# Kernel tuning notes

Measured on AMD Instinct MI355X. Metric: run time of the kernel, lower is better.

The kernel has to match this reference:

```python
import jax, jax.numpy as jnp
import numpy as np

BETA = 0.25


def setup_inputs() -> dict:
    key = jax.random.key(0)
    k1, k2, k3, k4 = jax.random.split(key, 4)
    B, D, T, H, W = 2, 256, 8, 32, 32
    K = 8192
    z = jax.random.normal(k1, (B, D, T, H, W), dtype=jnp.float32)
    # nn.init.normal_(embedding.weight, mean=0, std=emb_dim ** -0.5)
    emb_w = jax.random.normal(k2, (K, D), dtype=jnp.float32) * (D ** -0.5)
    # torch Linear default init ~ U(-1/sqrt(in), 1/sqrt(in)); scaled normal is fine for a reference
    w1 = jax.random.normal(k3, (D, D), dtype=jnp.float32) * (D ** -0.5)
    w2 = jax.random.normal(k4, (D, D), dtype=jnp.float32) * (D ** -0.5)
    return {"z": z, "emb_w": emb_w, "w1": w1, "w2": w2}


def reference(z, emb_w, w1, w2):
    B, D, T, H, W = z.shape
    K = emb_w.shape[0]
    # permute to channels-last and flatten: [B,T,H,W,D] -> [N,D]
    z_cl = jnp.transpose(z, (0, 2, 3, 4, 1))
    z_flat = z_cl.reshape(-1, D)
    N = z_flat.shape[0]
    # simvq: Linear -> GELU (exact) -> Linear, both bias-free
    quant_codebook = jax.nn.gelu(emb_w @ w1.T, approximate=False) @ w2.T  # [K, D]
    # pairwise squared L2 distances [N, K]
    d = (
        jnp.sum(z_flat ** 2, axis=1, keepdims=True)
        + jnp.sum(quant_codebook ** 2, axis=1)
        - 2.0 * (z_flat @ quant_codebook.T)
    )
    mean_distance = jnp.mean(d)
    idx = jnp.argmin(d, axis=1)  # [N]
    # gather == one-hot @ codebook
    z_q_flat = quant_codebook[idx]  # [N, D]
    z_q = z_q_flat.reshape(z_cl.shape)
    # VQ loss with stop-gradients
    loss = jnp.mean((jax.lax.stop_gradient(z_q) - z_cl) ** 2) + BETA * jnp.mean(
        (z_q - jax.lax.stop_gradient(z_cl)) ** 2
    )
    # straight-through estimator
    z_q = z_cl + jax.lax.stop_gradient(z_q - z_cl)
    # perplexity from code usage histogram (== mean of one-hot encodings)
    counts = jnp.zeros((K,), dtype=jnp.float32).at[idx].add(1.0)
    e_mean = counts / N
    perplexity = jnp.exp(-jnp.sum(e_mean * jnp.log(e_mean + 1e-10)))
    # back to channels-first [B, D, T, H, W]
    z_q = jnp.transpose(z_q, (0, 4, 1, 2, 3))
    return z_q, loss, perplexity, mean_distance
```

## Files before the change

kernel.cpp:

```cpp
#include <hip/hip_runtime.h>
#include <math.h>

#define BATCH 2
#define DIM   256
#define THW   8192
#define NTOK  16384
#define KCB   8192
#define OUTQ  4194304
#define CAP   2000000
#define SCAP  5600

typedef short short8 __attribute__((ext_vector_type(8)));
typedef float f32x4 __attribute__((ext_vector_type(4)));

__device__ __forceinline__ unsigned short f2bf_rn(float v) {
    unsigned u = __float_as_uint(v);
    unsigned r = u + 0x7FFFu + ((u >> 16) & 1u);
    return (unsigned short)(r >> 16);
}
__device__ __forceinline__ float bf2f(unsigned short b) {
    return __uint_as_float((unsigned)b << 16);
}
__device__ __forceinline__ void gl2lds16(const unsigned short* g, unsigned short* l) {
    __builtin_amdgcn_global_load_lds(
        (const __attribute__((address_space(1))) void*)g,
        (__attribute__((address_space(3))) void*)l, 16, 0, 0);
}

__global__ void k_buildA(const float* __restrict__ z,
                         unsigned short* __restrict__ Ahi,
                         unsigned short* __restrict__ Alo,
                         float* __restrict__ zsq,
                         float* __restrict__ sA, float* __restrict__ sB,
                         float* __restrict__ partialZ) {
    __shared__ ushort2 tile[64][65];
    __shared__ float zacc[64];
    __shared__ float lacc[64];
    __shared__ float pz[256];
    int t = threadIdx.x;
    int n0 = blockIdx.x * 64;
    int b = n0 >> 13;
    int thw0 = n0 & 8191;
    if (t < 64) { zacc[t] = 0.f; lacc[t] = 0.f; }
    pz[t] = 0.f;
    __syncthreads();
    int nn_r = t & 63, dg = t >> 6;
    float a1 = 0.f, a2 = 0.f;
    for (int dc = 0; dc < 256; dc += 64) {
        for (int r = 0; r < 16; ++r) {
            int dd = r * 4 + dg;
            float v = z[((size_t)(b * 256 + dc + dd)) * 8192 + thw0 + nn_r];
            unsigned short hb = f2bf_rn(v);
            float hf = bf2f(hb);
            unsigned short lb = f2bf_rn(v - hf);
            float lf = bf2f(lb);
            tile[dd][nn_r] = make_ushort2(hb, lb);
            a1 += v * v;
            a2 += lf * lf;
        }
        __syncthreads();
        int kk = t & 63, ng = t >> 6;
        float dimsum = 0.f;
        for (int i2 = 0; i2 < 16; ++i2) {
            int nn = ng + i2 * 4;
            ushort2 hl = tile[kk][nn];
            size_t base = (size_t)(n0 + nn) * 256;
            Ahi[base + dc + kk] = hl.x;
            Alo[base + dc + kk] = hl.y;
            dimsum += bf2f(hl.x) + bf2f(hl.y);
        }
        atomicAdd(&pz[dc + kk], dimsum);
        __syncthreads();
    }
    atomicAdd(&zacc[nn_r], a1);
    atomicAdd(&lacc[nn_r], a2);
    __syncthreads();
    if (t < 64) {
        zsq[n0 + t] = zacc[t];
        sA[n0 + t] = 2.1f * sqrtf(lacc[t]);
        sB[n0 + t] = 2.1f * sqrtf(zacc[t]);
    }
    partialZ[blockIdx.x * 256 + t] = pz[t];
}

__global__ void k_splitW(const float* __restrict__ w1, const float* __restrict__ w2,
                         unsigned short* __restrict__ W1s, unsigned short* __restrict__ W2s) {
    int bid = blockIdx.x;
    int row = bid & 255;
    const float* src = (bid >> 8) ? w2 : w1;
    unsigned short* dst = ((bid >> 8) ? W2s : W1s) + (size_t)row * 768;
    int t = threadIdx.x;
    float v = src[row * 256 + t];
    unsigned short hb = f2bf_rn(v);
    unsigned short lb = f2bf_rn(v - bf2f(hb));
    dst[t] = hb;
    dst[256 + t] = hb;
    dst[512 + t] = lb;
}

__global__ void k_buildE(const float* __restrict__ emb, unsigned short* __restrict__ E) {
    int t = threadIdx.x;
    int row = blockIdx.x * 4 + (t >> 6);
    int e4 = (t & 63) * 4;
    float4 v = *(const float4*)&emb[(size_t)row * 256 + e4];
    ushort4 hi, lo;
    hi.x = f2bf_rn(v.x); lo.x = f2bf_rn(v.x - bf2f(hi.x));
    hi.y = f2bf_rn(v.y); lo.y = f2bf_rn(v.y - bf2f(hi.y));
    hi.z = f2bf_rn(v.z); lo.z = f2bf_rn(v.z - bf2f(hi.z));
    hi.w = f2bf_rn(v.w); lo.w = f2bf_rn(v.w - bf2f(hi.w));
    size_t base = (size_t)row * 768;
    *(ushort4*)&E[base + e4] = hi;
    *(ushort4*)&E[base + 256 + e4] = lo;
    *(ushort4*)&E[base + 512 + e4] = hi;
}

template <int GELU>
__global__ __launch_bounds__(256) void k_mlp(const unsigned short* __restrict__ A,
                                             const unsigned short* __restrict__ B,
                                             unsigned short* __restrict__ Hs,
                                             float* __restrict__ C_t) {
    __shared__ __align__(16) char smem[32768];
    unsigned short* Asm = (unsigned short*)smem;
    unsigned short* Bsm = (unsigned short*)(smem + 16384);

    int t = threadIdx.x;
    int lane = t & 63;
    int w = t >> 6;
    int wm = w >> 1, wn = w & 1;
    int m0 = blockIdx.y * 128;
    int n0 = blockIdx.x * 128;

    int rA = w * 8 + (lane >> 3);
    int ch_l = lane & 7;
    int ch_g = ch_l ^ (lane >> 3);
    const unsigned short* gA = A + (size_t)(m0 + rA) * 768 + ch_g * 8;
    const unsigned short* gB = B + (size_t)(n0 + rA) * 768 + ch_g * 8;
    unsigned short* lA = &Asm[rA * 64 + ch_l * 8];
    unsigned short* lB = &Bsm[rA * 64 + ch_l * 8];

    f32x4 acc[4][4];
#pragma unroll
    for (int i = 0; i < 4; ++i)
#pragma unroll
        for (int j = 0; j < 4; ++j)
            acc[i][j] = f32x4{0.f, 0.f, 0.f, 0.f};

#pragma unroll
    for (int i = 0; i < 4; ++i) {
        gl2lds16(gA + (size_t)(32 * i) * 768, lA + 32 * i * 64);
        gl2lds16(gB + (size_t)(32 * i) * 768, lB + 32 * i * 64);
    }
    __syncthreads();

    int l15 = lane & 15;
    int quad = lane >> 4;
    int sw = l15 & 7;
    for (int kc = 0; kc < 12; ++kc) {
#pragma unroll
        for (int kk = 0; kk < 2; ++kk) {
            short8 a[4], b[4];
#pragma unroll
            for (int i = 0; i < 4; ++i)
                a[i] = *(const short8*)&Asm[(wm * 64 + i * 16 + l15) * 64 +
                                            (((kk * 4 + quad) ^ sw) * 8)];
#pragma unroll
            for (int j = 0; j < 4; ++j)
                b[j] = *(const short8*)&Bsm[(wn * 64 + j * 16 + l15) * 64 +
                                            (((kk * 4 + quad) ^ sw) * 8)];
#pragma unroll
            for (int i = 0; i < 4; ++i)
#pragma unroll
                for (int j = 0; j < 4; ++j)
                    acc[i][j] = __builtin_amdgcn_mfma_f32_16x16x32_bf16(a[i], b[j], acc[i][j], 0, 0, 0);
        }
        __syncthreads();
        if (kc < 11) {
            int ko = (kc + 1) * 64;
#pragma unroll
            for (int i = 0; i < 4; ++i) {
                gl2lds16(gA + (size_t)(32 * i) * 768 + ko, lA + 32 * i * 64);
                gl2lds16(gB + (size_t)(32 * i) * 768 + ko, lB + 32 * i * 64);
            }
            __syncthreads();
        }
    }

#pragma unroll
    for (int i = 0; i < 4; ++i) {
#pragma unroll
        for (int reg = 0; reg < 4; ++reg) {
            int mrow = m0 + wm * 64 + i * 16 + quad * 4 + reg;
#pragma unroll
            for (int j = 0; j < 4; ++j) {
                int ncol = n0 + wn * 64 + j * 16 + l15;
                float h = acc[i][j][reg];
                if (GELU) {
                    float g = 0.5f * h * (1.f + erff(h * 0.70710678118654752f));
                    unsigned short hb = f2bf_rn(g);
                    unsigned short lb = f2bf_rn(g - bf2f(hb));
                    size_t base = (size_t)mrow * 768;
                    Hs[base + ncol] = hb;
                    Hs[base + 256 + ncol] = lb;
                    Hs[base + 512 + ncol] = hb;
                } else {
                    C_t[(size_t)mrow * 8192 + ncol] = h;
                }
            }
        }
    }
}

__global__ void k_buildB(const float* __restrict__ C_t,
                         unsigned short* __restrict__ Bhi,
                         unsigned short* __restrict__ Blo,
                         float* __restrict__ csq,
                         float* __restrict__ sC, float* __restrict__ sCl,
                         unsigned* __restrict__ tileMaxC, unsigned* __restrict__ tileMaxCl,
                         float* __restrict__ accums, float* __restrict__ partialC) {
    __shared__ ushort2 tile[64][65];
    __shared__ float kacc[64];
    __shared__ float lacc[64];
    __shared__ float pc[256];
    int t = threadIdx.x;
    int k0 = blockIdx.x * 64;
    if (t < 64) { kacc[t] = 0.f; lacc[t] = 0.f; }
    pc[t] = 0.f;
    __syncthreads();
    int nn_r = t & 63, dg = t >> 6;
    float a1 = 0.f, a2 = 0.f;
    for (int dc = 0; dc < 256; dc += 64) {
        for (int r = 0; r < 16; ++r) {
            int dd = r * 4 + dg;
            float v = C_t[(size_t)(dc + dd) * KCB + k0 + nn_r];
            unsigned short hb = f2bf_rn(v);
            float hf = bf2f(hb);
            unsigned short lb = f2bf_rn(v - hf);
            float lf = bf2f(lb);
            tile[dd][nn_r] = make_ushort2(hb, lb);
            a1 += v * v;
            a2 += lf * lf;
        }
        __syncthreads();
        int kk = t & 63, ng = t >> 6;
        float dimsum = 0.f;
        for (int i2 = 0; i2 < 16; ++i2) {
            int nn = ng + i2 * 4;
            ushort2 hl = tile[kk][nn];
            size_t base = (size_t)(k0 + nn) * 256;
            Bhi[base + dc + kk] = hl.x;
            Blo[base + dc + kk] = hl.y;
            dimsum += bf2f(hl.x) + bf2f(hl.y);
        }
        atomicAdd(&pc[dc + kk], dimsum);
        __syncthreads();
    }
    atomicAdd(&kacc[nn_r], a1);
    atomicAdd(&lacc[nn_r], a2);
    __syncthreads();
    if (t < 64) {
        float c2 = kacc[t], l2 = lacc[t];
        float sc = sqrtf(c2), sl = sqrtf(l2);
        csq[k0 + t] = c2;
        sC[k0 + t] = sc;
        sCl[k0 + t] = sl;
        int tl = blockIdx.x >> 1;
        atomicMax(&tileMaxC[tl], __float_as_uint(sc));
        atomicMax(&tileMaxCl[tl], __float_as_uint(sl));
        atomicMax((unsigned*)&accums[3], __float_as_uint(c2));
        atomicMax((unsigned*)&accums[4], __float_as_uint(l2));
    }
    partialC[blockIdx.x * 256 + t] = pc[t];
}

__global__ __launch_bounds__(512, 2) void k_dist_hi(const unsigned short* __restrict__ A,
                                                    const unsigned short* __restrict__ B,
                                                    const float* __restrict__ zsq,
                                                    const float* __restrict__ csq,
                                                    const float* __restrict__ sA,
                                                    const float* __restrict__ sB,
                                                    const unsigned* __restrict__ tileMaxC,
                                                    const unsigned* __restrict__ tileMaxCl,
                                                    unsigned long long* __restrict__ packed,
                                                    float* __restrict__ accums,
                                                    unsigned long long* __restrict__ cand) {
    __shared__ __align__(16) char smem[131072];
    float* sbd     = (float*)smem;
    float* gprev_s = (float*)(smem + 2048);
    float* thr     = (float*)(smem + 3072);
    unsigned* scnt  = (unsigned*)(smem + 4096);
    unsigned* sbase = (unsigned*)(smem + 4100);
    unsigned long long* scand = (unsigned long long*)(smem + 4112);

    int t = threadIdx.x;
    int lane = t & 63;
    int w = t >> 6;
    int wm = w >> 1, wn = w & 1;
    int m0 = blockIdx.x * 256;
    int n0 = blockIdx.y * 256;

    int rA0 = w * 8 + (lane >> 3);
    int ch_l = lane & 7;
    int ch_g = ch_l ^ (lane >> 3);
    const unsigned short* gA = A + (size_t)(m0 + rA0) * 256 + ch_g * 8;
    const unsigned short* gB = B + (size_t)(n0 + rA0) * 256 + ch_g * 8;
    unsigned short* smemU = (unsigned short*)smem;
    unsigned short* lA = smemU + rA0 * 64 + ch_l * 8;
    unsigned short* lB = smemU + 16384 + rA0 * 64 + ch_l * 8;

    int l15 = lane & 15;
    int quad = lane >> 4;
    int sw = l15 & 7;

    float M1 = sqrtf(accums[3]);
    float M2 = sqrtf(accums[4]);
    float msC  = fmaxf(__uint_as_float(tileMaxC[2 * blockIdx.y]),
                       __uint_as_float(tileMaxC[2 * blockIdx.y + 1]));
    float msCl = fmaxf(__uint_as_float(tileMaxCl[2 * blockIdx.y]),
                       __uint_as_float(tileMaxCl[2 * blockIdx.y + 1]));
    float cv[8];
    int cols[8];
#pragma unroll
    for (int j = 0; j < 8; ++j) {
        int cloc = wn * 128 + j * 16 + l15;
        cols[j] = n0 + cloc;
        cv[j] = csq[cols[j]];
    }

    f32x4 acc[4][8];
#pragma unroll
    for (int i = 0; i < 4; ++i)
#pragma unroll
        for (int j = 0; j < 8; ++j)
            acc[i][j] = f32x4{0.f, 0.f, 0.f, 0.f};

#pragma unroll
    for (int i = 0; i < 4; ++i)
        gl2lds16(gA + (size_t)(64 * i) * 256, lA + 64 * i * 64);
#pragma unroll
    for (int i = 0; i < 4; ++i)
        gl2lds16(gB + (size_t)(64 * i) * 256, lB + 64 * i * 64);
    __syncthreads();

    int cur = 0;
    for (int kc = 0; kc < 4; ++kc) {
        if (kc < 3) {
            int ko = (kc + 1) * 64;
            int nb = (cur ^ 1) * 32768;
#pragma unroll
            for (int i = 0; i < 4; ++i)
                gl2lds16(gA + (size_t)(64 * i) * 256 + ko, lA + nb + 64 * i * 64);
#pragma unroll
            for (int i = 0; i < 4; ++i)
                gl2lds16(gB + (size_t)(64 * i) * 256 + ko, lB + nb + 64 * i * 64);
        }
        const unsigned short* Ar = smemU + cur * 32768;
        const unsigned short* Br = smemU + cur * 32768 + 16384;
#pragma unroll
        for (int kk = 0; kk < 2; ++kk) {
            short8 a[4], b[8];
#pragma unroll
            for (int i = 0; i < 4; ++i)
                a[i] = *(const short8*)&Ar[(wm * 64 + i * 16 + l15) * 64 +
                                            (((kk * 4 + quad) ^ sw) * 8)];
#pragma unroll
            for (int j = 0; j < 8; ++j)
                b[j] = *(const short8*)&Br[(wn * 128 + j * 16 + l15) * 64 +
                                            (((kk * 4 + quad) ^ sw) * 8)];
#pragma unroll
            for (int i = 0; i < 4; ++i)
#pragma unroll
                for (int j = 0; j < 8; ++j)
                    acc[i][j] = __builtin_amdgcn_mfma_f32_16x16x32_bf16(a[i], b[j], acc[i][j], 0, 0, 0);
        }
        __syncthreads();
        cur ^= 1;
    }

    if (t == 0) *scnt = 0;
    if (t < 256) {
        const unsigned* hp = (const unsigned*)&packed[m0 + t];
        gprev_s[t] = __uint_as_float(__atomic_load_n(hp + 1, __ATOMIC_RELAXED));
    }
#pragma unroll
    for (int i = 0; i < 4; ++i) {
#pragma unroll
        for (int reg = 0; reg < 4; ++reg) {
            int rloc = wm * 64 + i * 16 + quad * 4 + reg;
            float zs = zsq[m0 + rloc];
            float bd = 3.4e38f;
#pragma unroll
            for (int j = 0; j < 8; ++j) {
                float d = (zs + cv[j]) - 2.0f * acc[i][j][reg];
                acc[i][j][reg] = d;
                bd = fminf(bd, d);
            }
#pragma unroll
            for (int off = 1; off < 16; off <<= 1)
                bd = fminf(bd, __shfl_xor(bd, off, 64));
            if (l15 == 0) sbd[wn * 256 + rloc] = bd;
        }
    }
    __syncthreads();
    if (t < 256) {
        float bd = fminf(sbd[t], sbd[256 + t]);
        atomicMin(&packed[m0 + t], (unsigned long long)__float_as_uint(bd) << 32);
        float g = fminf(bd, gprev_s[t]);
        thr[t] = g + 1e-3f + sA[m0 + t] * (M1 + msC) + sB[m0 + t] * (M2 + msCl);
    }
    __syncthreads();
    unsigned* cnt = (unsigned*)&accums[2];
#pragma unroll
    for (int i = 0; i < 4; ++i) {
#pragma unroll
        for (int reg = 0; reg < 4; ++reg) {
            int rloc = wm * 64 + i * 16 + quad * 4 + reg;
            float tr = thr[rloc];
            bool p[8];
            bool any = false;
#pragma unroll
            for (int j = 0; j < 8; ++j) {
                p[j] = acc[i][j][reg] <= tr;
                any |= p[j];
            }
            if (__ballot(any)) {
                unsigned rbits = (unsigned)((m0 + rloc) << 13);
#pragma unroll
                for (int j = 0; j < 8; ++j) {
                    if (p[j]) {
                        unsigned long long entry =
                            ((unsigned long long)__float_as_uint(acc[i][j][reg]) << 32) |
                            (rbits | (unsigned)cols[j]);
                        unsigned pos = atomicAdd(scnt, 1u);
                        if (pos < SCAP) scand[pos] = entry;
                        else {
                            unsigned gp2 = atomicAdd(cnt, 1u);
                            if (gp2 < CAP) cand[gp2] = entry;
                        }
                    }
                }
            }
        }
    }
    __syncthreads();
    if (t == 0) {
        unsigned m = *scnt;
        if (m > SCAP) m = SCAP;
        *scnt = m;
        *sbase = atomicAdd(cnt, m);
    }
    __syncthreads();
    {
        unsigned m = *scnt, b0 = *sbase;
        for (unsigned u = t; u < m; u += 512)
            if (b0 + u < CAP) cand[b0 + u] = scand[u];
    }
}

__global__ __launch_bounds__(256) void k_rescore(const unsigned long long* __restrict__ cand,
                                                 const unsigned short* __restrict__ Ahi,
                                                 const unsigned short* __restrict__ Alo,
                                                 const unsigned short* __restrict__ Bhi,
                                                 const unsigned short* __restrict__ Blo,
                                                 const float* __restrict__ zsq,
                                                 const float* __restrict__ csq,
                                                 const float* __restrict__ sA,
                                                 const float* __restrict__ sB,
                                                 const float* __restrict__ sC,
                                                 const float* __restrict__ sCl,
                                                 const unsigned long long* __restrict__ packed,
                                                 unsigned long long* __restrict__ packed2,
                                                 const float* __restrict__ accums) {
    unsigned total = *(const unsigned*)&accums[2];
    if (total > CAP) total = CAP;
    float M1 = sqrtf(accums[3]);
    float M2 = sqrtf(accums[4]);
    int lane = threadIdx.x & 63;
    unsigned wv = blockIdx.x * 4 + (threadIdx.x >> 6);
    unsigned nw = gridDim.x * 4;
    for (unsigned e = wv; e < total; e += nw) {
        unsigned long long ent = cand[e];
        float dhi = __uint_as_float((unsigned)(ent >> 32));
        unsigned nk = (unsigned)ent;
        int n = (nk >> 13) & 16383;
        int k = nk & 8191;
        float g = __uint_as_float((unsigned)(packed[n] >> 32));
        float marg = g + 1e-3f + sA[n] * (M1 + sC[k]) + sB[n] * (M2 + sCl[k]);
        if (dhi > marg) continue;
        ushort4 zh = *((const ushort4*)(Ahi + (size_t)n * 256) + lane);
        ushort4 zl = *((const ushort4*)(Alo + (size_t)n * 256) + lane);
        ushort4 ch = *((const ushort4*)(Bhi + (size_t)k * 256) + lane);
        ushort4 cl = *((const ushort4*)(Blo + (size_t)k * 256) + lane);
        float s = (bf2f(zh.x) + bf2f(zl.x)) * (bf2f(ch.x) + bf2f(cl.x))
                + (bf2f(zh.y) + bf2f(zl.y)) * (bf2f(ch.y) + bf2f(cl.y))
                + (bf2f(zh.z) + bf2f(zl.z)) * (bf2f(ch.z) + bf2f(cl.z))
                + (bf2f(zh.w) + bf2f(zl.w)) * (bf2f(ch.w) + bf2f(cl.w));
#pragma unroll
        for (int off = 1; off < 64; off <<= 1)
            s += __shfl_xor(s, off, 64);
        if (lane == 0) {
            float dd = (zsq[n] + csq[k]) - 2.0f * s;
            unsigned long long p =
                ((unsigned long long)__float_as_uint(dd) << 32) | (unsigned)k;
            atomicMin(&packed2[n], p);
        }
    }
}

__global__ void k_unpack(const unsigned long long* __restrict__ packed2,
                         int* __restrict__ idx, int* __restrict__ counts) {
    int n = blockIdx.x * 256 + threadIdx.x;
    unsigned long long p = packed2[n];
    int k = (int)(p & 0xffffffffull);
    idx[n] = k;
    atomicAdd(&counts[k], 1);
}

__global__ void k_zqloss(const float* __restrict__ z, const float* __restrict__ C_t,
                         const int* __restrict__ idx, float* __restrict__ out,
                         float* __restrict__ loss_sum) {
    __shared__ float red[256];
    int bid = blockIdx.x;
    int b = bid >> 8;
    int d = bid & 255;
    int t = threadIdx.x;
    const float* crow = C_t + (size_t)d * KCB;
    const int* ib = idx + b * THW;
    size_t base = ((size_t)(b * DIM + d)) * THW;
    float lsum = 0.f;
    for (int it = 0; it < 32; ++it) {
        int thw = it * 256 + t;
        int id = ib[thw];
        float v = crow[id];
        float zz = z[base + thw];
        out[base + thw] = v;
        float df = v - zz;
        lsum += df * df;
    }
    red[t] = lsum;
    __syncthreads();
    for (int s = 128; s > 0; s >>= 1) {
        if (t < s) red[t] += red[t + s];
        __syncthreads();
    }
    if (t == 0) atomicAdd(loss_sum, red[0]);
}

__global__ void k_scalars(const int* __restrict__ counts,
                          const float* __restrict__ accums,
                          const float* __restrict__ zsq, const float* __restrict__ csq,
                          const float* __restrict__ partialZ,
                          const float* __restrict__ partialC,
                          float* __restrict__ out_tail) {
    __shared__ double redd[256];
    __shared__ float redf[256];
    int t = threadIdx.x;
    double szsq = 0.0, scsq = 0.0;
    for (int n = t; n < NTOK; n += 256) szsq += (double)zsq[n];
    for (int k = t; k < KCB; k += 256) scsq += (double)csq[k];
    float SZ = 0.f, SC = 0.f;
    for (int b2 = 0; b2 < 256; ++b2) SZ += partialZ[b2 * 256 + t];
    for (int b2 = 0; b2 < 128; ++b2) SC += partialC[b2 * 256 + t];
    double total = 8192.0 * szsq + 16384.0 * scsq - 2.0 * (double)SZ * (double)SC;
    redd[t] = total;
    float s = 0.f;
    for (int k = t; k < KCB; k += 256) {
        float e = (float)counts[k] * (1.0f / 16384.0f);
        s += e * logf(e + 1e-10f);
    }
    redf[t] = s;
    __syncthreads();
    for (int st = 128; st > 0; st >>= 1) {
        if (t < st) { redd[t] += redd[t + st]; redf[t] += redf[t + st]; }
        __syncthreads();
    }
    if (t == 0) {
        out_tail[0] = 1.25f * accums[1] / 4194304.0f;
        out_tail[1] = expf(-redf[0]);
        out_tail[2] = (float)(redd[0] / (16384.0 * 8192.0));
    }
}

extern "C" void kernel_launch(void* const* d_in, const int* in_sizes, int n_in,
                              void* d_out, int out_size, void* d_ws, size_t ws_size,
                              hipStream_t stream) {
    const float* z     = (const float*)d_in[0];
    const float* emb_w = (const float*)d_in[1];
    const float* w1    = (const float*)d_in[2];
    const float* w2    = (const float*)d_in[3];
    float* out = (float*)d_out;

    char* w = (char*)d_ws;
    unsigned short* Ahi = (unsigned short*)(w + 0);
    unsigned short* Alo = (unsigned short*)(w + 8388608);
    unsigned short* Ebf = (unsigned short*)(w + 16777216);
    unsigned short* Bhi = (unsigned short*)(w + 29360128);
    unsigned short* Blo = (unsigned short*)(w + 33554432);
    unsigned short* W1s = (unsigned short*)(w + 37748736);
    unsigned short* W2s = (unsigned short*)(w + 38141952);
    float* zsq   = (float*)(w + 38535168);
    float* sA    = (float*)(w + 38666240);
    float* sB    = (float*)(w + 38731776);
    float* csq   = (float*)(w + 38797312);
    float* sC    = (float*)(w + 38862848);
    float* sCl   = (float*)(w + 38895616);
    unsigned long long* packed  = (unsigned long long*)(w + 38928384);
    unsigned long long* packed2 = (unsigned long long*)(w + 39059456);
    int*   idx    = (int*)(w + 39190528);
    int*   counts = (int*)(w + 39256064);
    float* partialZ = (float*)(w + 39288832);
    float* partialC = (float*)(w + 39550976);
    unsigned* tileMaxC  = (unsigned*)(w + 39682048);
    unsigned* tileMaxCl = (unsigned*)(w + 39682304);
    float* accums = (float*)(w + 39682560);

    float* C_t = (float*)Ebf;
    unsigned short* Hs = (unsigned short*)d_out;
    unsigned long long* cand = (unsigned long long*)d_out;

    hipMemsetAsync(counts, 0, 32768, stream);
    hipMemsetAsync(tileMaxC, 0, 1024, stream);
    hipMemsetAsync(packed, 0xFF, 262144, stream);

    k_buildA<<<NTOK / 64, 256, 0, stream>>>(z, Ahi, Alo, zsq, sA, sB, partialZ);
    k_splitW<<<512, 256, 0, stream>>>(w1, w2, W1s, W2s);
    k_buildE<<<KCB / 4, 256, 0, stream>>>(emb_w, Ebf);

    k_mlp<1><<<dim3(2, KCB / 128), 256, 0, stream>>>(Ebf, W1s, Hs, nullptr);
    k_mlp<0><<<dim3(KCB / 128, 2), 256, 0, stream>>>(W2s, Hs, nullptr, C_t);

    k_buildB<<<KCB / 64, 256, 0, stream>>>(C_t, Bhi, Blo, csq, sC, sCl,
                                           tileMaxC, tileMaxCl, accums, partialC);

    k_dist_hi<<<dim3(NTOK / 256, KCB / 256), 512, 0, stream>>>(
        Ahi, Bhi, zsq, csq, sA, sB, tileMaxC, tileMaxCl, packed, accums, cand);

    k_rescore<<<1024, 256, 0, stream>>>(cand, Ahi, Alo, Bhi, Blo, zsq, csq,
                                        sA, sB, sC, sCl, packed, packed2, accums);

    k_unpack<<<NTOK / 256, 256, 0, stream>>>(packed2, idx, counts);
    k_zqloss<<<BATCH * DIM, 256, 0, stream>>>(z, C_t, idx, out, accums + 1);
    k_scalars<<<1, 256, 0, stream>>>(counts, accums, zsq, csq, partialZ, partialC, out + OUTQ);
}
```

Measured before the change: 393.3 us.

## Triple-buffer k_dist_hi GEMM with smaller K chunks and XCD-aware tile remap

Restructures the main distance GEMM in k_dist_hi from a 2-stage, 64-wide K-chunk loop into a fully unrolled 3-stage pipeline over 32-wide K chunks. It uses explicit vmcnt waits, raw barriers and s_setprio around the MFMA bursts. Blocks are remapped so that tiles scheduled on the same XCD share A/B rows for L2 locality. LDS per block shrinks from 128KB to 96KB, and the csq loads move after the GEMM to cut register pressure. The risk is more barriers per K, plus correctness depending on the hand-tuned waitcnt and the swizzle.

```diff
diff --git a/kernel.cpp b/kernel.cpp
--- a/kernel.cpp
+++ b/kernel.cpp
@@ -283,7 +283,7 @@
                                                     unsigned long long* __restrict__ packed,
                                                     float* __restrict__ accums,
                                                     unsigned long long* __restrict__ cand) {
-    __shared__ __align__(16) char smem[131072];
+    __shared__ __align__(16) char smem[98304];
     float* sbd     = (float*)smem;
     float* gprev_s = (float*)(smem + 2048);
     float* thr     = (float*)(smem + 3072);
@@ -295,28 +295,92 @@
     int lane = t & 63;
     int w = t >> 6;
     int wm = w >> 1, wn = w & 1;
-    int m0 = blockIdx.x * 256;
-    int n0 = blockIdx.y * 256;
-
-    int rA0 = w * 8 + (lane >> 3);
-    int ch_l = lane & 7;
-    int ch_g = ch_l ^ (lane >> 3);
-    const unsigned short* gA = A + (size_t)(m0 + rA0) * 256 + ch_g * 8;
-    const unsigned short* gB = B + (size_t)(n0 + rA0) * 256 + ch_g * 8;
+
+    unsigned f = blockIdx.x + (blockIdx.y << 6);
+    unsigned xcd = f & 7, i5 = f >> 3;
+    unsigned mb = (xcd & 3) * 16 + (i5 & 15);
+    unsigned nb = (xcd >> 2) * 16 + (i5 >> 4);
+    int m0 = (int)mb * 256;
+    int n0 = (int)nb * 256;
+
+    int rsrow = t >> 2;
+    int rch = (t & 3) ^ (rsrow & 3);
+    const unsigned short* gA0 = A + (size_t)(m0 + rsrow) * 256 + rch * 8;
+    const unsigned short* gB0 = B + (size_t)(n0 + rsrow) * 256 + rch * 8;
     unsigned short* smemU = (unsigned short*)smem;
-    unsigned short* lA = smemU + rA0 * 64 + ch_l * 8;
-    unsigned short* lB = smemU + 16384 + rA0 * 64 + ch_l * 8;
 
     int l15 = lane & 15;
     int quad = lane >> 4;
-    int sw = l15 & 7;
+    int sw2 = l15 & 3;
 
     float M1 = sqrtf(accums[3]);
     float M2 = sqrtf(accums[4]);
-    float msC  = fmaxf(__uint_as_float(tileMaxC[2 * blockIdx.y]),
-                       __uint_as_float(tileMaxC[2 * blockIdx.y + 1]));
-    float msCl = fmaxf(__uint_as_float(tileMaxCl[2 * blockIdx.y]),
-                       __uint_as_float(tileMaxCl[2 * blockIdx.y + 1]));
+    float msC  = fmaxf(__uint_as_float(tileMaxC[2 * nb]),
+                       __uint_as_float(tileMaxC[2 * nb + 1]));
+    float msCl = fmaxf(__uint_as_float(tileMaxCl[2 * nb]),
+                       __uint_as_float(tileMaxCl[2 * nb + 1]));
+
+    f32x4 acc[4][8];
+#pragma unroll
+    for (int i = 0; i < 4; ++i)
+#pragma unroll
+        for (int j = 0; j < 8; ++j)
+            acc[i][j] = f32x4{0.f, 0.f, 0.f, 0.f};
+
+#define STAGE(b, koff)                                                      \
+    {                                                                       \
+        unsigned short* base_ = smemU + (b) * 16384;                        \
+        gl2lds16(gA0 + (koff), base_ + t * 8);                              \
+        gl2lds16(gA0 + 128 * 256 + (koff), base_ + 4096 + t * 8);           \
+        gl2lds16(gB0 + (koff), base_ + 8192 + t * 8);                       \
+        gl2lds16(gB0 + 128 * 256 + (koff), base_ + 12288 + t * 8);          \
+    }
+
+#define KSTEP(KC, BUF, WN, DOSTAGE)                                         \
+    {                                                                       \
+        __builtin_amdgcn_sched_barrier(0);                                  \
+        __builtin_amdgcn_s_barrier();   \
+        __builtin_amdgcn_sched_barrier(0);                                  \
+        if (DOSTAGE) STAGE(((KC) + 2) % 3, ((KC) + 2) * 32);                \
+        asm volatile("s_waitcnt vmcnt(" #WN ")" ::: "memory");              \
+        __builtin_amdgcn_sched_barrier(0);                                  \
+        __builtin_amdgcn_s_barrier();           \
+        __builtin_amdgcn_sched_barrier(0);                                  \
+        const unsigned short* Ar = smemU + (BUF) * 16384;                   \
+        const unsigned short* Br = Ar + 8192;                               \
+        short8 a[4], b[8];                                                  \
+        _Pragma("unroll")                                                   \
+        for (int i = 0; i < 4; ++i)                                         \
+            a[i] = *(const short8*)&Ar[(wm * 64 + i * 16 + l15) * 32 +      \
+                                       ((quad ^ sw2) * 8)];                 \
+        _Pragma("unroll")                                                   \
+        for (int j = 0; j < 8; ++j)                                         \
+            b[j] = *(const short8*)&Br[(wn * 128 + j * 16 + l15) * 32 +     \
+                                       ((quad ^ sw2) * 8)];                 \
+        __builtin_amdgcn_s_setprio(1);                                      \
+        _Pragma("unroll")                                                   \
+        for (int i = 0; i < 4; ++i)                                         \
+            _Pragma("unroll")                                               \
+            for (int j = 0; j < 8; ++j)                                     \
+                acc[i][j] = __builtin_amdgcn_mfma_f32_16x16x32_bf16(        \
+                    a[i], b[j], acc[i][j], 0, 0, 0);                        \
+        __builtin_amdgcn_s_setprio(0);                                      \
+    }
+
+    STAGE(0, 0)
+    STAGE(1, 32)
+    KSTEP(0, 0, 8, 1)
+    KSTEP(1, 1, 8, 1)
+    KSTEP(2, 2, 8, 1)
+    KSTEP(3, 0, 8, 1)
+    KSTEP(4, 1, 8, 1)
+    KSTEP(5, 2, 8, 1)
+    KSTEP(6, 0, 4, 0)
+    KSTEP(7, 1, 0, 0)
+#undef KSTEP
+#undef STAGE
+    __syncthreads();
+
     float cv[8];
     int cols[8];
 #pragma unroll
@@ -324,56 +388,6 @@
         int cloc = wn * 128 + j * 16 + l15;
         cols[j] = n0 + cloc;
         cv[j] = csq[cols[j]];
-    }
-
-    f32x4 acc[4][8];
-#pragma unroll
-    for (int i = 0; i < 4; ++i)
-#pragma unroll
-        for (int j = 0; j < 8; ++j)
-            acc[i][j] = f32x4{0.f, 0.f, 0.f, 0.f};
-
-#pragma unroll
-    for (int i = 0; i < 4; ++i)
-        gl2lds16(gA + (size_t)(64 * i) * 256, lA + 64 * i * 64);
-#pragma unroll
-    for (int i = 0; i < 4; ++i)
-        gl2lds16(gB + (size_t)(64 * i) * 256, lB + 64 * i * 64);
-    __syncthreads();
-
-    int cur = 0;
-    for (int kc = 0; kc < 4; ++kc) {
-        if (kc < 3) {
-            int ko = (kc + 1) * 64;
-            int nb = (cur ^ 1) * 32768;
-#pragma unroll
-            for (int i = 0; i < 4; ++i)
-                gl2lds16(gA + (size_t)(64 * i) * 256 + ko, lA + nb + 64 * i * 64);
-#pragma unroll
-            for (int i = 0; i < 4; ++i)
-                gl2lds16(gB + (size_t)(64 * i) * 256 + ko, lB + nb + 64 * i * 64);
-        }
-        const unsigned short* Ar = smemU + cur * 32768;
-        const unsigned short* Br = smemU + cur * 32768 + 16384;
-#pragma unroll
-        for (int kk = 0; kk < 2; ++kk) {
-            short8 a[4], b[8];
-#pragma unroll
-            for (int i = 0; i < 4; ++i)
-                a[i] = *(const short8*)&Ar[(wm * 64 + i * 16 + l15) * 64 +
-                                            (((kk * 4 + quad) ^ sw) * 8)];
-#pragma unroll
-            for (int j = 0; j < 8; ++j)
-                b[j] = *(const short8*)&Br[(wn * 128 + j * 16 + l15) * 64 +
-                                            (((kk * 4 + quad) ^ sw) * 8)];
-#pragma unroll
-            for (int i = 0; i < 4; ++i)
-#pragma unroll
-                for (int j = 0; j < 8; ++j)
-                    acc[i][j] = __builtin_amdgcn_mfma_f32_16x16x32_bf16(a[i], b[j], acc[i][j], 0, 0, 0);
-        }
-        __syncthreads();
-        cur ^= 1;
     }
 
     if (t == 0) *scnt = 0;
```

Measured after the change: 401.7 us. 1.02x slower.

## Remap dist tiles per XCD, split codebook into two launches, warp-aggregate candidate appends

Applied to the files above, without the earlier changes.

Block indices in the distance kernel are remapped so that each of the 8 XCDs works on a compact 16x8 patch of M and N tiles, which should improve L2 reuse of A and B rows. The kernel is launched twice, once for each half of the codebook. The second launch then sees tighter running minima in packed, which may reduce the number of candidates. Candidate appends to shared memory now use one ballot plus one atomic per wave instead of one atomic per thread. The csq loads are also moved after the GEMM. In exchange there is an extra launch and a serialization point between the two halves.

```diff
diff --git a/kernel.cpp b/kernel.cpp
--- a/kernel.cpp
+++ b/kernel.cpp
@@ -282,6 +282,7 @@
                                                     const unsigned* __restrict__ tileMaxCl,
                                                     unsigned long long* __restrict__ packed,
                                                     float* __restrict__ accums,
+                                                    int nhalf,
                                                     unsigned long long* __restrict__ cand) {
     __shared__ __align__(16) char smem[131072];
     float* sbd     = (float*)smem;
@@ -295,8 +296,13 @@
     int lane = t & 63;
     int w = t >> 6;
     int wm = w >> 1, wn = w & 1;
-    int m0 = blockIdx.x * 256;
-    int n0 = blockIdx.y * 256;
+
+    unsigned f = blockIdx.x + (blockIdx.y << 6);
+    unsigned xcd = f & 7, i5 = f >> 3;
+    unsigned mb = (xcd & 3) * 16 + (i5 & 15);
+    unsigned nb = (unsigned)nhalf * 16 + (xcd >> 2) * 8 + (i5 >> 4);
+    int m0 = (int)mb * 256;
+    int n0 = (int)nb * 256;
 
     int rA0 = w * 8 + (lane >> 3);
     int ch_l = lane & 7;
@@ -313,10 +319,61 @@
 
     float M1 = sqrtf(accums[3]);
     float M2 = sqrtf(accums[4]);
-    float msC  = fmaxf(__uint_as_float(tileMaxC[2 * blockIdx.y]),
-                       __uint_as_float(tileMaxC[2 * blockIdx.y + 1]));
-    float msCl = fmaxf(__uint_as_float(tileMaxCl[2 * blockIdx.y]),
-                       __uint_as_float(tileMaxCl[2 * blockIdx.y + 1]));
+    float msC  = fmaxf(__uint_as_float(tileMaxC[2 * nb]),
+                       __uint_as_float(tileMaxC[2 * nb + 1]));
+    float msCl = fmaxf(__uint_as_float(tileMaxCl[2 * nb]),
+                       __uint_as_float(tileMaxCl[2 * nb + 1]));
+
+    f32x4 acc[4][8];
+#pragma unroll
+    for (int i = 0; i < 4; ++i)
+#pragma unroll
+        for (int j = 0; j < 8; ++j)
+            acc[i][j] = f32x4{0.f, 0.f, 0.f, 0.f};
+
+#define STAGE(B_, KO)                                                       \
+    {                                                                       \
+        int off_ = (B_) * 32768;                                            \
+        _Pragma("unroll")                                                   \
+        for (int i_ = 0; i_ < 4; ++i_)                                      \
+            gl2lds16(gA + (size_t)(64 * i_) * 256 + (KO),                   \
+                     lA + off_ + 64 * i_ * 64);                             \
+        _Pragma("unroll")                                                   \
+        for (int i_ = 0; i_ < 4; ++i_)                                      \
+            gl2lds16(gB + (size_t)(64 * i_) * 256 + (KO),                   \
+                     lB + off_ + 64 * i_ * 64);                             \
+    }
+
+    STAGE(0, 0)
+    __syncthreads();
+
+    int cur = 0;
+    for (int kc = 0; kc < 4; ++kc) {
+        if (kc < 3) STAGE(cur ^ 1, (kc + 1) * 64)
+        const unsigned short* Ar = smemU + cur * 32768;
+        const unsigned short* Br = Ar + 16384;
+#pragma unroll
+        for (int kk = 0; kk < 2; ++kk) {
+            short8 a[4], b[8];
+#pragma unroll
+            for (int i = 0; i < 4; ++i)
+                a[i] = *(const short8*)&Ar[(wm * 64 + i * 16 + l15) * 64 +
+                                            (((kk * 4 + quad) ^ sw) * 8)];
+#pragma unroll
+            for (int j = 0; j < 8; ++j)
+                b[j] = *(const short8*)&Br[(wn * 128 + j * 16 + l15) * 64 +
+                                            (((kk * 4 + quad) ^ sw) * 8)];
+#pragma unroll
+            for (int i = 0; i < 4; ++i)
+#pragma unroll
+                for (int j = 0; j < 8; ++j)
+                    acc[i][j] = __builtin_amdgcn_mfma_f32_16x16x32_bf16(a[i], b[j], acc[i][j], 0, 0, 0);
+        }
+        __syncthreads();
+        cur ^= 1;
+    }
+#undef STAGE
+
     float cv[8];
     int cols[8];
 #pragma unroll
@@ -324,56 +381,6 @@
         int cloc = wn * 128 + j * 16 + l15;
         cols[j] = n0 + cloc;
         cv[j] = csq[cols[j]];
-    }
-
-    f32x4 acc[4][8];
-#pragma unroll
-    for (int i = 0; i < 4; ++i)
-#pragma unroll
-        for (int j = 0; j < 8; ++j)
-            acc[i][j] = f32x4{0.f, 0.f, 0.f, 0.f};
-
-#pragma unroll
-    for (int i = 0; i < 4; ++i)
-        gl2lds16(gA + (size_t)(64 * i) * 256, lA + 64 * i * 64);
-#pragma unroll
-    for (int i = 0; i < 4; ++i)
-        gl2lds16(gB + (size_t)(64 * i) * 256, lB + 64 * i * 64);
-    __syncthreads();
-
-    int cur = 0;
-    for (int kc = 0; kc < 4; ++kc) {
-        if (kc < 3) {
-            int ko = (kc + 1) * 64;
-            int nb = (cur ^ 1) * 32768;
-#pragma unroll
-            for (int i = 0; i < 4; ++i)
-                gl2lds16(gA + (size_t)(64 * i) * 256 + ko, lA + nb + 64 * i * 64);
-#pragma unroll
-            for (int i = 0; i < 4; ++i)
-                gl2lds16(gB + (size_t)(64 * i) * 256 + ko, lB + nb + 64 * i * 64);
-        }
-        const unsigned short* Ar = smemU + cur * 32768;
-        const unsigned short* Br = smemU + cur * 32768 + 16384;
-#pragma unroll
-        for (int kk = 0; kk < 2; ++kk) {
-            short8 a[4], b[8];
-#pragma unroll
-            for (int i = 0; i < 4; ++i)
-                a[i] = *(const short8*)&Ar[(wm * 64 + i * 16 + l15) * 64 +
-                                            (((kk * 4 + quad) ^ sw) * 8)];
-#pragma unroll
-            for (int j = 0; j < 8; ++j)
-                b[j] = *(const short8*)&Br[(wn * 128 + j * 16 + l15) * 64 +
-                                            (((kk * 4 + quad) ^ sw) * 8)];
-#pragma unroll
-            for (int i = 0; i < 4; ++i)
-#pragma unroll
-                for (int j = 0; j < 8; ++j)
-                    acc[i][j] = __builtin_amdgcn_mfma_f32_16x16x32_bf16(a[i], b[j], acc[i][j], 0, 0, 0);
-        }
-        __syncthreads();
-        cur ^= 1;
     }
 
     if (t == 0) *scnt = 0;
@@ -415,22 +422,22 @@
         for (int reg = 0; reg < 4; ++reg) {
             int rloc = wm * 64 + i * 16 + quad * 4 + reg;
             float tr = thr[rloc];
-            bool p[8];
-            bool any = false;
+            unsigned rbits = (unsigned)((m0 + rloc) << 13);
 #pragma unroll
             for (int j = 0; j < 8; ++j) {
-                p[j] = acc[i][j][reg] <= tr;
-                any |= p[j];
-            }
-            if (__ballot(any)) {
-                unsigned rbits = (unsigned)((m0 + rloc) << 13);
-#pragma unroll
-                for (int j = 0; j < 8; ++j) {
-                    if (p[j]) {
+                bool p = acc[i][j][reg] <= tr;
+                unsigned long long mask = __ballot(p);
+                if (mask) {
+                    unsigned cw = (unsigned)__popcll(mask);
+                    unsigned base;
+                    if (lane == 0) base = atomicAdd(scnt, cw);
+                    base = __shfl(base, 0, 64);
+                    if (p) {
+                        unsigned pos = base +
+                            (unsigned)__popcll(mask & ((1ull << lane) - 1ull));
                         unsigned long long entry =
                             ((unsigned long long)__float_as_uint(acc[i][j][reg]) << 32) |
                             (rbits | (unsigned)cols[j]);
-                        unsigned pos = atomicAdd(scnt, 1u);
                         if (pos < SCAP) scand[pos] = entry;
                         else {
                             unsigned gp2 = atomicAdd(cnt, 1u);
@@ -631,8 +638,10 @@
     k_buildB<<<KCB / 64, 256, 0, stream>>>(C_t, Bhi, Blo, csq, sC, sCl,
                                            tileMaxC, tileMaxCl, accums, partialC);
 
-    k_dist_hi<<<dim3(NTOK / 256, KCB / 256), 512, 0, stream>>>(
-        Ahi, Bhi, zsq, csq, sA, sB, tileMaxC, tileMaxCl, packed, accums, cand);
+    k_dist_hi<<<dim3(64, 16), 512, 0, stream>>>(
+        Ahi, Bhi, zsq, csq, sA, sB, tileMaxC, tileMaxCl, packed, accums, 0, cand);
+    k_dist_hi<<<dim3(64, 16), 512, 0, stream>>>(
+        Ahi, Bhi, zsq, csq, sA, sB, tileMaxC, tileMaxCl, packed, accums, 1, cand);
 
     k_rescore<<<1024, 256, 0, stream>>>(cand, Ahi, Alo, Bhi, Blo, zsq, csq,
                                         sA, sB, sC, sCl, packed, packed2, accums);
```

Result: slower. 444.0 us (+12.9%).

## Fold memsets and unpack into existing kernels, vectorize zq gather, atomic partial sums

Applied to the files above, without the earlier changes.

Removes three hipMemsetAsync calls by zeroing counts, tile maxima, accums and partial buffers inside k_splitW (now launched first) and initializing packed/packed2 inside k_buildA. Drops k_unpack by having k_zqloss read indices directly from packed2 with vectorized loads, with the d==0 blocks building the histogram. Per-block partial dim sums become atomicAdds into one 256-entry vector, so k_scalars no longer loops over blocks. This trims launch count and tail-kernel work, at the cost of atomic contention and some extra serialized counting in a subset of blocks.

```diff
diff --git a/kernel.cpp b/kernel.cpp
--- a/kernel.cpp
+++ b/kernel.cpp
@@ -27,12 +27,43 @@
         (__attribute__((address_space(3))) void*)l, 16, 0, 0);
 }
 
+__global__ void k_splitW(const float* __restrict__ w1, const float* __restrict__ w2,
+                         unsigned short* __restrict__ W1s, unsigned short* __restrict__ W2s,
+                         int* __restrict__ counts,
+                         unsigned* __restrict__ tileMaxC, unsigned* __restrict__ tileMaxCl,
+                         float* __restrict__ accums,
+                         float* __restrict__ partialZ, float* __restrict__ partialC) {
+    int bid = blockIdx.x;
+    int t = threadIdx.x;
+    if (bid < 32) {
+        counts[bid * 256 + t] = 0;
+    } else if (bid == 32) {
+        if (t < 64) { tileMaxC[t] = 0u; tileMaxCl[t] = 0u; }
+        if (t >= 64 && t < 72) accums[t - 64] = 0.f;
+    } else if (bid == 33) {
+        partialZ[t] = 0.f;
+    } else if (bid == 34) {
+        partialC[t] = 0.f;
+    }
+    int row = bid & 255;
+    const float* src = (bid >> 8) ? w2 : w1;
+    unsigned short* dst = ((bid >> 8) ? W2s : W1s) + (size_t)row * 768;
+    float v = src[row * 256 + t];
+    unsigned short hb = f2bf_rn(v);
+    unsigned short lb = f2bf_rn(v - bf2f(hb));
+    dst[t] = hb;
+    dst[256 + t] = hb;
+    dst[512 + t] = lb;
+}
+
 __global__ void k_buildA(const float* __restrict__ z,
                          unsigned short* __restrict__ Ahi,
                          unsigned short* __restrict__ Alo,
                          float* __restrict__ zsq,
                          float* __restrict__ sA, float* __restrict__ sB,
-                         float* __restrict__ partialZ) {
+                         float* __restrict__ partialZ,
+                         unsigned long long* __restrict__ packed,
+                         unsigned long long* __restrict__ packed2) {
     __shared__ ushort2 tile[64][65];
     __shared__ float zacc[64];
     __shared__ float lacc[64];
@@ -41,7 +72,11 @@
     int n0 = blockIdx.x * 64;
     int b = n0 >> 13;
     int thw0 = n0 & 8191;
-    if (t < 64) { zacc[t] = 0.f; lacc[t] = 0.f; }
+    if (t < 64) {
+        zacc[t] = 0.f; lacc[t] = 0.f;
+        packed[n0 + t] = ~0ull;
+        packed2[n0 + t] = ~0ull;
+    }
     pz[t] = 0.f;
     __syncthreads();
     int nn_r = t & 63, dg = t >> 6;
@@ -80,22 +115,7 @@
         sA[n0 + t] = 2.1f * sqrtf(lacc[t]);
         sB[n0 + t] = 2.1f * sqrtf(zacc[t]);
     }
-    partialZ[blockIdx.x * 256 + t] = pz[t];
-}
-
-__global__ void k_splitW(const float* __restrict__ w1, const float* __restrict__ w2,
-                         unsigned short* __restrict__ W1s, unsigned short* __restrict__ W2s) {
-    int bid = blockIdx.x;
-    int row = bid & 255;
-    const float* src = (bid >> 8) ? w2 : w1;
-    unsigned short* dst = ((bid >> 8) ? W2s : W1s) + (size_t)row * 768;
-    int t = threadIdx.x;
-    float v = src[row * 256 + t];
-    unsigned short hb = f2bf_rn(v);
-    unsigned short lb = f2bf_rn(v - bf2f(hb));
-    dst[t] = hb;
-    dst[256 + t] = hb;
-    dst[512 + t] = lb;
+    atomicAdd(&partialZ[t], pz[t]);
 }
 
 __global__ void k_buildE(const float* __restrict__ emb, unsigned short* __restrict__ E) {
@@ -269,7 +289,7 @@
         atomicMax((unsigned*)&accums[3], __float_as_uint(c2));
         atomicMax((unsigned*)&accums[4], __float_as_uint(l2));
     }
-    partialC[blockIdx.x * 256 + t] = pc[t];
+    atomicAdd(&partialC[t], pc[t]);
 }
 
 __global__ __launch_bounds__(512, 2) void k_dist_hi(const unsigned short* __restrict__ A,
@@ -333,28 +353,27 @@
         for (int j = 0; j < 8; ++j)
             acc[i][j] = f32x4{0.f, 0.f, 0.f, 0.f};
 
-#pragma unroll
-    for (int i = 0; i < 4; ++i)
-        gl2lds16(gA + (size_t)(64 * i) * 256, lA + 64 * i * 64);
-#pragma unroll
-    for (int i = 0; i < 4; ++i)
-        gl2lds16(gB + (size_t)(64 * i) * 256, lB + 64 * i * 64);
+#define STAGE(B_, KO)                                                       \
+    {                                                                       \
+        int off_ = (B_) * 32768;                                            \
+        _Pragma("unroll")                                                   \
+        for (int i_ = 0; i_ < 4; ++i_)                                      \
+            gl2lds16(gA + (size_t)(64 * i_) * 256 + (KO),                   \
+                     lA + off_ + 64 * i_ * 64);                             \
+        _Pragma("unroll")                                                   \
+        for (int i_ = 0; i_ < 4; ++i_)                                      \
+            gl2lds16(gB + (size_t)(64 * i_) * 256 + (KO),                   \
+                     lB + off_ + 64 * i_ * 64);                             \
+    }
+
+    STAGE(0, 0)
     __syncthreads();
 
     int cur = 0;
     for (int kc = 0; kc < 4; ++kc) {
-        if (kc < 3) {
-            int ko = (kc + 1) * 64;
-            int nb = (cur ^ 1) * 32768;
-#pragma unroll
-            for (int i = 0; i < 4; ++i)
-                gl2lds16(gA + (size_t)(64 * i) * 256 + ko, lA + nb + 64 * i * 64);
-#pragma unroll
-            for (int i = 0; i < 4; ++i)
-                gl2lds16(gB + (size_t)(64 * i) * 256 + ko, lB + nb + 64 * i * 64);
-        }
+        if (kc < 3) STAGE(cur ^ 1, (kc + 1) * 64)
         const unsigned short* Ar = smemU + cur * 32768;
-        const unsigned short* Br = smemU + cur * 32768 + 16384;
+        const unsigned short* Br = Ar + 16384;
 #pragma unroll
         for (int kk = 0; kk < 2; ++kk) {
             short8 a[4], b[8];
@@ -375,6 +394,7 @@
         __syncthreads();
         cur ^= 1;
     }
+#undef STAGE
 
     if (t == 0) *scnt = 0;
     if (t < 256) {
@@ -506,35 +526,39 @@
     }
 }
 
-__global__ void k_unpack(const unsigned long long* __restrict__ packed2,
-                         int* __restrict__ idx, int* __restrict__ counts) {
-    int n = blockIdx.x * 256 + threadIdx.x;
-    unsigned long long p = packed2[n];
-    int k = (int)(p & 0xffffffffull);
-    idx[n] = k;
-    atomicAdd(&counts[k], 1);
-}
-
 __global__ void k_zqloss(const float* __restrict__ z, const float* __restrict__ C_t,
-                         const int* __restrict__ idx, float* __restrict__ out,
-                         float* __restrict__ loss_sum) {
+                         const unsigned long long* __restrict__ packed2,
+                         float* __restrict__ out, float* __restrict__ loss_sum,
+                         int* __restrict__ counts) {
     __shared__ float red[256];
     int bid = blockIdx.x;
     int b = bid >> 8;
     int d = bid & 255;
     int t = threadIdx.x;
     const float* crow = C_t + (size_t)d * KCB;
-    const int* ib = idx + b * THW;
+    const unsigned long long* pb = packed2 + (size_t)b * THW;
     size_t base = ((size_t)(b * DIM + d)) * THW;
     float lsum = 0.f;
-    for (int it = 0; it < 32; ++it) {
-        int thw = it * 256 + t;
-        int id = ib[thw];
-        float v = crow[id];
-        float zz = z[base + thw];
-        out[base + thw] = v;
-        float df = v - zz;
-        lsum += df * df;
+    for (int it = 0; it < 8; ++it) {
+        int thw = it * 1024 + t * 4;
+        ulonglong2 p01 = *(const ulonglong2*)&pb[thw];
+        ulonglong2 p23 = *(const ulonglong2*)&pb[thw + 2];
+        int i0 = (int)(unsigned)p01.x & 8191;
+        int i1 = (int)(unsigned)p01.y & 8191;
+        int i2 = (int)(unsigned)p23.x & 8191;
+        int i3 = (int)(unsigned)p23.y & 8191;
+        float4 zz = *(const float4*)&z[base + thw];
+        float4 v;
+        v.x = crow[i0]; v.y = crow[i1]; v.z = crow[i2]; v.w = crow[i3];
+        *(float4*)&out[base + thw] = v;
+        float d0 = v.x - zz.x, d1 = v.y - zz.y, d2 = v.z - zz.z, d3 = v.w - zz.w;
+        lsum += d0 * d0 + d1 * d1 + d2 * d2 + d3 * d3;
+        if (d == 0) {
+            atomicAdd(&counts[i0], 1);
+            atomicAdd(&counts[i1], 1);
+            atomicAdd(&counts[i2], 1);
+            atomicAdd(&counts[i3], 1);
+        }
     }
     red[t] = lsum;
     __syncthreads();
@@ -557,9 +581,8 @@
     double szsq = 0.0, scsq = 0.0;
     for (int n = t; n < NTOK; n += 256) szsq += (double)zsq[n];
     for (int k = t; k < KCB; k += 256) scsq += (double)csq[k];
-    float SZ = 0.f, SC = 0.f;
-    for (int b2 = 0; b2 < 256; ++b2) SZ += partialZ[b2 * 256 + t];
-    for (int b2 = 0; b2 < 128; ++b2) SC += partialC[b2 * 256 + t];
+    float SZ = partialZ[t];
+    float SC = partialC[t];
     double total = 8192.0 * szsq + 16384.0 * scsq - 2.0 * (double)SZ * (double)SC;
     redd[t] = total;
     float s = 0.f;
@@ -605,7 +628,6 @@
     float* sCl   = (float*)(w + 38895616);
     unsigned long long* packed  = (unsigned long long*)(w + 38928384);
     unsigned long long* packed2 = (unsigned long long*)(w + 39059456);
-    int*   idx    = (int*)(w + 39190528);
     int*   counts = (int*)(w + 39256064);
     float* partialZ = (float*)(w + 39288832);
     float* partialC = (float*)(w + 39550976);
@@ -617,12 +639,10 @@
     unsigned short* Hs = (unsigned short*)d_out;
     unsigned long long* cand = (unsigned long long*)d_out;
 
-    hipMemsetAsync(counts, 0, 32768, stream);
-    hipMemsetAsync(tileMaxC, 0, 1024, stream);
-    hipMemsetAsync(packed, 0xFF, 262144, stream);
-
-    k_buildA<<<NTOK / 64, 256, 0, stream>>>(z, Ahi, Alo, zsq, sA, sB, partialZ);
-    k_splitW<<<512, 256, 0, stream>>>(w1, w2, W1s, W2s);
+    k_splitW<<<512, 256, 0, stream>>>(w1, w2, W1s, W2s, counts,
+                                      tileMaxC, tileMaxCl, accums, partialZ, partialC);
+    k_buildA<<<NTOK / 64, 256, 0, stream>>>(z, Ahi, Alo, zsq, sA, sB, partialZ,
+                                            packed, packed2);
     k_buildE<<<KCB / 4, 256, 0, stream>>>(emb_w, Ebf);
 
     k_mlp<1><<<dim3(2, KCB / 128), 256, 0, stream>>>(Ebf, W1s, Hs, nullptr);
@@ -637,7 +657,6 @@
     k_rescore<<<1024, 256, 0, stream>>>(cand, Ahi, Alo, Bhi, Blo, zsq, csq,
                                         sA, sB, sC, sCl, packed, packed2, accums);
 
-    k_unpack<<<NTOK / 256, 256, 0, stream>>>(packed2, idx, counts);
-    k_zqloss<<<BATCH * DIM, 256, 0, stream>>>(z, C_t, idx, out, accums + 1);
+    k_zqloss<<<BATCH * DIM, 256, 0, stream>>>(z, C_t, packed2, out, accums + 1, counts);
     k_scalars<<<1, 256, 0, stream>>>(counts, accums, zsq, csq, partialZ, partialC, out + OUTQ);
 }
```

Result: slower. 411.4 us (+4.6%).
